# Kernel tuning notes

Measured on AMD Instinct MI355X. Metric: run time of the kernel, lower is better.

The kernel has to match this reference:

```python
import jax, jax.numpy as jnp
import numpy as np

SIGMA = 1.0
BN_EPS = 1e-5
N_OP, N_MACH, N_JOB = 200000, 1000, 20000
E_OM, E_JO, N_PAIRS = 1000000, 200000, 500000
H, D0 = 64, 32


def _bn(x, g, b):
    # BatchNorm1d, training-mode batch statistics over the node/row dim
    m = x.mean(0)
    v = x.var(0)
    return g * (x - m) * jax.lax.rsqrt(v + BN_EPS) + b


def _encode(x, W):
    # MultiPeriodicEncoder: learned frequencies, concat(sin, cos) -> 2*16 = 32 dims
    h = (x @ W) / SIGMA
    return jnp.concatenate([jnp.sin(h), jnp.cos(h)], axis=-1)


def _gin(x_dst, agg, eps, W1, b1, g1, be1, W2, b2):
    # GINConv: MLP((1+eps)*x + sum-aggregated messages); MLP = Lin->BN->ReLU->Lin
    h = ((1.0 + eps) * x_dst + agg) @ W1 + b1
    h = jax.nn.relu(_bn(h, g1, be1))
    return h @ W2 + b2


def _forward(x_operation, x_machine, x_job,
             W_enc_op, W_enc_mach, W_enc_job,
             gin_W1_l0, gin_W1_l12, gin_b1, gin_g1, gin_be1, gin_W2, gin_b2, gin_eps,
             Ws1, bs1, gs1, bes1, Ws2, bs2, gs2, bes2, Ws3, bs3,
             e_om_src, e_om_dst, e_mo_src, e_mo_dst, e_jo_src, e_jo_dst,
             e_oj_src, e_oj_dst, vp_op, vp_mach, vp_job):
    x_op = _encode(x_operation, W_enc_op)    # [N_OP, 32]
    x_ma = _encode(x_machine, W_enc_mach)    # [N_MACH, 32]
    x_jb = _encode(x_job, W_enc_job)         # [N_JOB, 32]
    num_layers = gin_eps.shape[0]
    for l in range(num_layers):
        def p(e):
            W1 = gin_W1_l0[e] if l == 0 else gin_W1_l12[l - 1, e]
            return (gin_eps[l, e], W1, gin_b1[l, e], gin_g1[l, e],
                    gin_be1[l, e], gin_W2[l, e], gin_b2[l, e])
        # edge-type order: 0=op->mach, 1=mach->op, 2=job->op, 3=op->job
        agg_mach = jax.ops.segment_sum(x_op[e_om_src], e_om_dst, num_segments=N_MACH)
        agg_op_mo = jax.ops.segment_sum(x_ma[e_mo_src], e_mo_dst, num_segments=N_OP)
        agg_op_jo = jax.ops.segment_sum(x_jb[e_jo_src], e_jo_dst, num_segments=N_OP)
        agg_job = jax.ops.segment_sum(x_op[e_oj_src], e_oj_dst, num_segments=N_JOB)
        new_ma = _gin(x_ma, agg_mach, *p(0))
        new_op = _gin(x_op, agg_op_mo, *p(1)) + _gin(x_op, agg_op_jo, *p(2))  # hetero 'sum'
        new_jb = _gin(x_jb, agg_job, *p(3))
        if l > 0:  # residual add of previous layer output (= current input)
            new_op = new_op + x_op
            new_ma = new_ma + x_ma
            new_jb = new_jb + x_jb
        x_op, x_ma, x_jb = new_op, new_ma, new_jb
    # gather by valid_pairs, concat in node-type order [operation, machine, job]
    feat = jnp.concatenate([x_op[vp_op], x_ma[vp_mach], x_jb[vp_job]], axis=1)  # [P, 192]
    h = jax.nn.relu(_bn(feat @ Ws1 + bs1, gs1, bes1))
    h = jax.nn.relu(_bn(h @ Ws2 + bs2, gs2, bes2))
    return (h @ Ws3 + bs3)[:, 0]


def setup_inputs() -> dict:
    key = jax.random.key(0)
    ks = jax.random.split(key, 24)
    rn = lambda k, s: jax.random.normal(k, s, dtype=jnp.float32) * 0.1
    return {
        'x_operation': jax.random.normal(ks[0], (N_OP, 8), dtype=jnp.float32),
        'x_machine': jax.random.normal(ks[1], (N_MACH, 4), dtype=jnp.float32),
        'x_job': jax.random.normal(ks[2], (N_JOB, 4), dtype=jnp.float32),
        'W_enc_op': rn(ks[3], (8, 16)),
        'W_enc_mach': rn(ks[4], (4, 16)),
        'W_enc_job': rn(ks[5], (4, 16)),
        'gin_W1_l0': rn(ks[6], (4, D0, H)),
        'gin_W1_l12': rn(ks[7], (2, 4, H, H)),
        'gin_b1': jnp.zeros((3, 4, H), jnp.float32),
        'gin_g1': jnp.ones((3, 4, H), jnp.float32),
        'gin_be1': jnp.zeros((3, 4, H), jnp.float32),
        'gin_W2': rn(ks[8], (3, 4, H, H)),
        'gin_b2': jnp.zeros((3, 4, H), jnp.float32),
        'gin_eps': jnp.zeros((3, 4), jnp.float32),
        'Ws1': rn(ks[9], (3 * H, H)),
        'bs1': jnp.zeros((H,), jnp.float32),
        'gs1': jnp.ones((H,), jnp.float32),
        'bes1': jnp.zeros((H,), jnp.float32),
        'Ws2': rn(ks[10], (H, H // 2)),
        'bs2': jnp.zeros((H // 2,), jnp.float32),
        'gs2': jnp.ones((H // 2,), jnp.float32),
        'bes2': jnp.zeros((H // 2,), jnp.float32),
        'Ws3': rn(ks[11], (H // 2, 1)),
        'bs3': jnp.zeros((1,), jnp.float32),
        'e_om_src': jax.random.randint(ks[12], (E_OM,), 0, N_OP),
        'e_om_dst': jax.random.randint(ks[13], (E_OM,), 0, N_MACH),
        'e_mo_src': jax.random.randint(ks[14], (E_OM,), 0, N_MACH),
        'e_mo_dst': jax.random.randint(ks[15], (E_OM,), 0, N_OP),
        'e_jo_src': jax.random.randint(ks[16], (E_JO,), 0, N_JOB),
        'e_jo_dst': jax.random.randint(ks[17], (E_JO,), 0, N_OP),
        'e_oj_src': jax.random.randint(ks[18], (E_JO,), 0, N_OP),
        'e_oj_dst': jax.random.randint(ks[19], (E_JO,), 0, N_JOB),
        'vp_op': jax.random.randint(ks[20], (N_PAIRS,), 0, N_OP),
        'vp_mach': jax.random.randint(ks[21], (N_PAIRS,), 0, N_MACH),
        'vp_job': jax.random.randint(ks[22], (N_PAIRS,), 0, N_JOB),
    }


def reference(x_operation, x_machine, x_job,
              W_enc_op, W_enc_mach, W_enc_job,
              gin_W1_l0, gin_W1_l12, gin_b1, gin_g1, gin_be1, gin_W2, gin_b2, gin_eps,
              Ws1, bs1, gs1, bes1, Ws2, bs2, gs2, bes2, Ws3, bs3,
              e_om_src, e_om_dst, e_mo_src, e_mo_dst, e_jo_src, e_jo_dst,
              e_oj_src, e_oj_dst, vp_op, vp_mach, vp_job):
    return _forward(x_operation, x_machine, x_job,
                    W_enc_op, W_enc_mach, W_enc_job,
                    gin_W1_l0, gin_W1_l12, gin_b1, gin_g1, gin_be1, gin_W2, gin_b2, gin_eps,
                    Ws1, bs1, gs1, bes1, Ws2, bs2, gs2, bes2, Ws3, bs3,
                    e_om_src, e_om_dst, e_mo_src, e_mo_dst, e_jo_src, e_jo_dst,
                    e_oj_src, e_oj_dst, vp_op, vp_mach, vp_job)
```

## Files before the change

kernel.cpp:

```cpp
#include <hip/hip_runtime.h>
#include <math.h>

#define N_OP_   200000
#define N_MACH_ 1000
#define N_JOB_  20000
#define E_OM_   1000000
#define E_JO_   200000
#define N_PAIRS_ 500000

#define B_OM_ 0
#define B_MO_ 64000
#define B_JO_ 264000
#define B_OJ_ 464000
#define TOTC_ 484000
#define E_TOT_ 2400000

#define CDIV(a,b) (((a)+(b)-1)/(b))

__device__ __forceinline__ unsigned short f2bf(float f){
  unsigned int u = __float_as_uint(f);
  return (unsigned short)((u + 0x7fffu + ((u>>16)&1u)) >> 16);
}
__device__ __forceinline__ float bf2f(unsigned short h){
  return __uint_as_float(((unsigned int)h)<<16);
}

template<int DIN>
__global__ __launch_bounds__(256) void encode_kernel(const float* __restrict__ x,
    const float* __restrict__ W, float* __restrict__ out, int N){
  __shared__ float sW[DIN*16];
  if (threadIdx.x < DIN*16) sW[threadIdx.x] = W[threadIdx.x];
  __syncthreads();
  int i = blockIdx.x*blockDim.x + threadIdx.x;
  if (i >= N) return;
  float xv[DIN];
#pragma unroll
  for (int k=0;k<DIN;k++) xv[k] = x[i*DIN+k];
#pragma unroll
  for (int j=0;j<16;j++){
    float h = 0.f;
#pragma unroll
    for (int k=0;k<DIN;k++) h = fmaf(xv[k], sW[k*16+j], h);
    float s, c;
    sincosf(h, &s, &c);
    out[(size_t)i*64 + j]      = s;
    out[(size_t)i*64 + 16 + j] = c;
  }
}

__device__ __forceinline__ int edge_cidx(int e,
    const int* __restrict__ eom_d, const int* __restrict__ emo_d,
    const int* __restrict__ ejo_d, const int* __restrict__ eoj_d){
  if (e < E_OM_)            return B_OM_ + eom_d[e]*64 + (e & 63);
  else if (e < 2*E_OM_)     return B_MO_ + emo_d[e - E_OM_];
  else if (e < 2*E_OM_+E_JO_) return B_JO_ + ejo_d[e - 2*E_OM_];
  else                      return B_OJ_ + eoj_d[e - 2*E_OM_ - E_JO_];
}
__device__ __forceinline__ int edge_src(int e,
    const int* __restrict__ eom_s, const int* __restrict__ emo_s,
    const int* __restrict__ ejo_s, const int* __restrict__ eoj_s){
  if (e < E_OM_)            return eom_s[e];
  else if (e < 2*E_OM_)     return emo_s[e - E_OM_];
  else if (e < 2*E_OM_+E_JO_) return ejo_s[e - 2*E_OM_];
  else                      return eoj_s[e - 2*E_OM_ - E_JO_];
}

__global__ __launch_bounds__(256) void hist_all_kernel(
    const int* __restrict__ eom_d, const int* __restrict__ emo_d,
    const int* __restrict__ ejo_d, const int* __restrict__ eoj_d,
    int* __restrict__ cnt){
  int gsz = gridDim.x*blockDim.x;
  int i0 = blockIdx.x*blockDim.x + threadIdx.x;
  for (int base = i0; base < E_TOT_; base += 8*gsz){
    int c[8]; bool act[8];
#pragma unroll
    for (int j=0;j<8;j++){
      int e = base + j*gsz;
      act[j] = (e < E_TOT_);
      if (act[j]) c[j] = edge_cidx(e, eom_d, emo_d, ejo_d, eoj_d);
    }
#pragma unroll
    for (int j=0;j<8;j++) if (act[j]) atomicAdd(&cnt[c[j]], 1);
  }
}

__global__ __launch_bounds__(256) void fill_all_kernel(
    const int* __restrict__ eom_s, const int* __restrict__ eom_d,
    const int* __restrict__ emo_s, const int* __restrict__ emo_d,
    const int* __restrict__ ejo_s, const int* __restrict__ ejo_d,
    const int* __restrict__ eoj_s, const int* __restrict__ eoj_d,
    int* __restrict__ cursor, int* __restrict__ elist){
  int gsz = gridDim.x*blockDim.x;
  int i0 = blockIdx.x*blockDim.x + threadIdx.x;
  for (int base = i0; base < E_TOT_; base += 8*gsz){
    int cidx[8], src[8]; bool act[8];
#pragma unroll
    for (int j=0;j<8;j++){
      int e = base + j*gsz;
      act[j] = (e < E_TOT_);
      if (act[j]){
        cidx[j] = edge_cidx(e, eom_d, emo_d, ejo_d, eoj_d);
        src[j]  = edge_src (e, eom_s, emo_s, ejo_s, eoj_s);
      }
    }
    int p[8];
#pragma unroll
    for (int j=0;j<8;j++) if (act[j]) p[j] = atomicAdd(&cursor[cidx[j]], 1);
#pragma unroll
    for (int j=0;j<8;j++) if (act[j]) elist[p[j]] = src[j];
  }
}

__global__ void scan_block_sums(const int* __restrict__ cnt, int N, int* __restrict__ partials){
  __shared__ int red[256];
  int base = blockIdx.x*2048;
  int s = 0;
#pragma unroll
  for (int j=0;j<8;j++){ int i = base + threadIdx.x + j*256; if (i<N) s += cnt[i]; }
  red[threadIdx.x] = s; __syncthreads();
  for (int st=128; st>0; st>>=1){ if (threadIdx.x<st) red[threadIdx.x]+=red[threadIdx.x+st]; __syncthreads(); }
  if (threadIdx.x==0) partials[blockIdx.x] = red[0];
}

__global__ void scan_partials(int* __restrict__ partials, int NB, int* __restrict__ offN){
  __shared__ int buf[256];
  int v = (threadIdx.x < NB) ? partials[threadIdx.x] : 0;
  buf[threadIdx.x] = v; __syncthreads();
  int acc = v;
  for (int st=1; st<256; st<<=1){
    int t = (threadIdx.x >= st) ? buf[threadIdx.x-st] : 0;
    __syncthreads();
    acc += t; buf[threadIdx.x] = acc;
    __syncthreads();
  }
  if (threadIdx.x < NB) partials[threadIdx.x] = acc - v;
  if (threadIdx.x == NB-1) offN[0] = acc;
}

__global__ void scan_write_offsets(const int* __restrict__ cnt, int N,
    const int* __restrict__ partials, int* __restrict__ off){
  __shared__ int buf[256];
  int base = blockIdx.x*2048;
  int v[8]; int s = 0;
#pragma unroll
  for (int j=0;j<8;j++){ int i = base + threadIdx.x*8 + j; v[j] = (i<N)?cnt[i]:0; s += v[j]; }
  buf[threadIdx.x] = s; __syncthreads();
  int acc = s;
  for (int st=1; st<256; st<<=1){
    int t = (threadIdx.x >= st) ? buf[threadIdx.x-st] : 0;
    __syncthreads();
    acc += t; buf[threadIdx.x] = acc;
    __syncthreads();
  }
  int ex = partials[blockIdx.x] + acc - s;
#pragma unroll
  for (int j=0;j<8;j++){ int i = base + threadIdx.x*8 + j; if (i<N) off[i] = ex; ex += v[j]; }
}

__global__ __launch_bounds__(256) void agg_block_kernel(const int* __restrict__ off,
    const int* __restrict__ srcs, const float* __restrict__ feat,
    float* __restrict__ outp, int Ndst, int D){
  __shared__ float red[4][64];
  int m = blockIdx.x;
  if (m >= Ndst) return;
  int g = threadIdx.x >> 6, lane = threadIdx.x & 63;
  int s = off[m*64], e = off[m*64 + 64];
  float acc = 0.f;
  for (int base = s + g*64; base < e; base += 256){
    int cnt = e - base; if (cnt > 64) cnt = 64;
    int r = (lane < cnt) ? srcs[base + lane] : 0;
    int i = 0;
    for (; i + 4 <= cnt; i += 4){
      int r0 = __shfl(r, i), r1 = __shfl(r, i+1), r2 = __shfl(r, i+2), r3 = __shfl(r, i+3);
      float v0 = feat[(size_t)r0*64 + lane];
      float v1 = feat[(size_t)r1*64 + lane];
      float v2 = feat[(size_t)r2*64 + lane];
      float v3 = feat[(size_t)r3*64 + lane];
      acc += (v0 + v1) + (v2 + v3);
    }
    for (; i < cnt; i++){
      int ri = __shfl(r, i);
      acc += feat[(size_t)ri*64 + lane];
    }
  }
  red[g][lane] = acc;
  __syncthreads();
  if (g==0 && lane<D)
    outp[(size_t)m*64+lane] = red[0][lane]+red[1][lane]+red[2][lane]+red[3][lane];
}

template<int K>
__global__ __launch_bounds__(256,3) void partA_fused_kernel(
    const int* __restrict__ off_all, const int* __restrict__ elist,
    const float* __restrict__ Xop, const float* __restrict__ Xma, const float* __restrict__ Xjb,
    float* hm, float* ho1, float* ho2, float* hj,
    const float* __restrict__ Wm, const float* __restrict__ Wa,
    const float* __restrict__ Wb, const float* __restrict__ Wj,
    const float* __restrict__ bm, const float* __restrict__ ba,
    const float* __restrict__ bb, const float* __restrict__ bj,
    float* __restrict__ lstats,
    const float* __restrict__ epsp, int ebase)
{
  constexpr int KP = K + 4;
  constexpr int NF4 = K/16;
  __shared__ float sW[K][64];
  __shared__ float sZ[64][KP];
  __shared__ float sred[16][64];
  const int tid = threadIdx.x;
  const int lc = tid & 15, lr = tid >> 4;
  const int Tm = (N_MACH_+63)>>6, To = (N_OP_+63)>>6;
  int t = blockIdx.x;
  int seg, tile;
  if (t < Tm){ seg=0; tile=t; }
  else if (t < Tm+To){ seg=1; tile=t-Tm; }
  else if (t < Tm+2*To){ seg=2; tile=t-Tm-To; }
  else { seg=3; tile=t-Tm-2*To; }
  float* z            = seg==0?hm:seg==1?ho1:seg==2?ho2:hj;
  const float* x      = seg==0?Xma:seg==3?Xjb:Xop;
  const float* feat   = seg==0?Xop:seg==1?Xma:seg==2?Xjb:Xop;
  const float* W      = seg==0?Wm:seg==1?Wa:seg==2?Wb:Wj;
  const float* b      = seg==0?bm:seg==1?ba:seg==2?bb:bj;
  const int N         = seg==0?N_MACH_:seg==3?N_JOB_:N_OP_;
  const int* offs     = off_all + (seg==0?B_OM_:seg==1?B_MO_:seg==2?B_JO_:B_OJ_);
  float* st           = lstats + seg*128;
  const float e1 = 1.0f + epsp[ebase + seg];
  for (int idx = tid*4; idx < K*64; idx += 1024){
    int k = idx >> 6, c = idx & 63;
    *(float4*)&sW[k][c] = *(const float4*)&W[(size_t)k*64 + c];
  }
  float4 bias4 = *(const float4*)&b[lc*4];
  const int rbase = tile << 6;
  {
    const int r = tid >> 2, q = tid & 3;
    const int cbase = q*(K/4);
    int row = rbase + r;
    float4 a4[NF4];
#pragma unroll
    for (int f=0; f<NF4; f++) a4[f] = make_float4(0.f,0.f,0.f,0.f);
    if (row < N){
      if (seg == 0){
        const float4* H4 = (const float4*)&z[(size_t)row*64 + cbase];
#pragma unroll
        for (int f=0; f<NF4; f++) a4[f] = H4[f];
      } else {
        int s = offs[row], e = offs[row+1];
        int i = s;
        for (; i+2<=e; i+=2){
          int s0 = elist[i], s1 = elist[i+1];
          const float4* F0 = (const float4*)&feat[(size_t)s0*64 + cbase];
          const float4* F1 = (const float4*)&feat[(size_t)s1*64 + cbase];
          float4 v0[NF4], v1[NF4];
#pragma unroll
          for (int f=0; f<NF4; f++){ v0[f]=F0[f]; v1[f]=F1[f]; }
#pragma unroll
          for (int f=0; f<NF4; f++){
            a4[f].x += v0[f].x + v1[f].x;
            a4[f].y += v0[f].y + v1[f].y;
            a4[f].z += v0[f].z + v1[f].z;
            a4[f].w += v0[f].w + v1[f].w;
          }
        }
        if (i < e){
          int s0 = elist[i];
          const float4* F0 = (const float4*)&feat[(size_t)s0*64 + cbase];
#pragma unroll
          for (int f=0; f<NF4; f++){
            float4 v = F0[f];
            a4[f].x += v.x; a4[f].y += v.y; a4[f].z += v.z; a4[f].w += v.w;
          }
        }
      }
      const float4* X4 = (const float4*)&x[(size_t)row*64 + cbase];
#pragma unroll
      for (int f=0; f<NF4; f++){
        float4 xv = X4[f];
        a4[f].x = fmaf(e1, xv.x, a4[f].x);
        a4[f].y = fmaf(e1, xv.y, a4[f].y);
        a4[f].z = fmaf(e1, xv.z, a4[f].z);
        a4[f].w = fmaf(e1, xv.w, a4[f].w);
      }
    }
#pragma unroll
    for (int f=0; f<NF4; f++) *(float4*)&sZ[r][cbase + f*4] = a4[f];
  }
  __syncthreads();
  float acc[4][4];
#pragma unroll
  for (int i=0;i<4;i++){ acc[i][0]=0.f; acc[i][1]=0.f; acc[i][2]=0.f; acc[i][3]=0.f; }
#pragma unroll 2
  for (int kb = 0; kb < K/4; kb++){
    float4 zf[4], wf[4];
#pragma unroll
    for (int i=0;i<4;i++) zf[i] = *(const float4*)&sZ[lr*4+i][kb*4];
#pragma unroll
    for (int kk=0;kk<4;kk++) wf[kk] = *(const float4*)&sW[kb*4+kk][lc*4];
#pragma unroll
    for (int i=0;i<4;i++){
      acc[i][0] = fmaf(zf[i].x, wf[0].x, acc[i][0]);
      acc[i][1] = fmaf(zf[i].x, wf[0].y, acc[i][1]);
      acc[i][2] = fmaf(zf[i].x, wf[0].z, acc[i][2]);
      acc[i][3] = fmaf(zf[i].x, wf[0].w, acc[i][3]);
      acc[i][0] = fmaf(zf[i].y, wf[1].x, acc[i][0]);
      acc[i][1] = fmaf(zf[i].y, wf[1].y, acc[i][1]);
      acc[i][2] = fmaf(zf[i].y, wf[1].z, acc[i][2]);
      acc[i][3] = fmaf(zf[i].y, wf[1].w, acc[i][3]);
      acc[i][0] = fmaf(zf[i].z, wf[2].x, acc[i][0]);
      acc[i][1] = fmaf(zf[i].z, wf[2].y, acc[i][1]);
      acc[i][2] = fmaf(zf[i].z, wf[2].z, acc[i][2]);
      acc[i][3] = fmaf(zf[i].z, wf[2].w, acc[i][3]);
      acc[i][0] = fmaf(zf[i].w, wf[3].x, acc[i][0]);
      acc[i][1] = fmaf(zf[i].w, wf[3].y, acc[i][1]);
      acc[i][2] = fmaf(zf[i].w, wf[3].z, acc[i][2]);
      acc[i][3] = fmaf(zf[i].w, wf[3].w, acc[i][3]);
    }
  }
  float4 psum = make_float4(0.f,0.f,0.f,0.f), psq = make_float4(0.f,0.f,0.f,0.f);
#pragma unroll
  for (int i=0;i<4;i++){
    int row = rbase + lr*4 + i;
    if (row < N){
      float4 o;
      o.x = acc[i][0] + bias4.x;
      o.y = acc[i][1] + bias4.y;
      o.z = acc[i][2] + bias4.z;
      o.w = acc[i][3] + bias4.w;
      *(float4*)&z[(size_t)row*64 + lc*4] = o;
      psum.x += o.x; psum.y += o.y; psum.z += o.z; psum.w += o.w;
      psq.x += o.x*o.x; psq.y += o.y*o.y; psq.z += o.z*o.z; psq.w += o.w*o.w;
    }
  }
  __syncthreads();
  *(float4*)&sred[lr][lc*4] = psum;
  __syncthreads();
  if (tid < 64){
    float s = 0.f;
#pragma unroll
    for (int j=0;j<16;j++) s += sred[j][tid];
    atomicAdd(&st[tid], s);
  }
  __syncthreads();
  *(float4*)&sred[lr][lc*4] = psq;
  __syncthreads();
  if (tid < 64){
    float s = 0.f;
#pragma unroll
    for (int j=0;j<16;j++) s += sred[j][tid];
    atomicAdd(&st[64+tid], s);
  }
}

template<bool RESID>
__global__ __launch_bounds__(256,3) void partB_batch_kernel(
    float* h0, const float* x0, const float* W20, const float* b20, const float* sc0, int N0,
    float* hA, const float* hBp, const float* x1, const float* W2a, const float* W2b,
    const float* b2a_, const float* b2b_, const float* scA, const float* scB, int N1,
    float* h3, const float* x3, const float* W23, const float* b23, const float* sc3, int N3)
{
  __shared__ float sW[64][64];
  __shared__ float sZ[64][68];
  const int tid = threadIdx.x;
  const int lc = tid & 15, lr = tid >> 4;
  const int T0=(N0+63)>>6, T1=(N1+63)>>6;
  int t = blockIdx.x;
  int seg, tile;
  if (t < T0){ seg=0; tile=t; }
  else if (t < T0+T1){ seg=1; tile=t-T0; }
  else { seg=2; tile=t-T0-T1; }
  const int N = seg==0?N0:seg==1?N1:N3;
  float* hout = seg==0?h0:seg==1?hA:h3;
  const float* x = seg==0?x0:seg==1?x1:x3;
  const int rbase = tile << 6;
  const int nsrc = (seg==1) ? 2 : 1;
  float4 bias4;
  if (seg==1){
    float4 ba4 = *(const float4*)&b2a_[lc*4];
    float4 bb4 = *(const float4*)&b2b_[lc*4];
    bias4 = make_float4(ba4.x+bb4.x, ba4.y+bb4.y, ba4.z+bb4.z, ba4.w+bb4.w);
  } else {
    const float* b = seg==0?b20:b23;
    bias4 = *(const float4*)&b[lc*4];
  }
  float acc[4][4];
#pragma unroll
  for (int i=0;i<4;i++){ acc[i][0]=0.f; acc[i][1]=0.f; acc[i][2]=0.f; acc[i][3]=0.f; }
  for (int s=0; s<nsrc; s++){
    const float* hsrc = (seg==1) ? (s==0? (const float*)hA : hBp)
                                 : (seg==0? (const float*)h0 : (const float*)h3);
    const float* Wp   = (seg==1) ? (s==0? W2a : W2b) : (seg==0? W20 : W23);
    const float* scp  = (seg==1) ? (s==0? scA : scB) : (seg==0? sc0 : sc3);
    __syncthreads();
    for (int idx = tid*4; idx < 4096; idx += 1024){
      int k = idx >> 6, c = idx & 63;
      *(float4*)&sW[k][c] = *(const float4*)&Wp[(size_t)k*64 + c];
    }
    for (int idx = tid*4; idx < 4096; idx += 1024){
      int r = idx >> 6, c = idx & 63;
      int row = rbase + r;
      float4 zv = make_float4(0.f,0.f,0.f,0.f);
      if (row < N){
        float4 hv = *(const float4*)&hsrc[(size_t)row*64 + c];
        float4 sc4 = *(const float4*)&scp[c];
        float4 sh4 = *(const float4*)&scp[64 + c];
        zv.x = fmaf(sc4.x, hv.x, sh4.x); zv.x = zv.x > 0.f ? zv.x : 0.f;
        zv.y = fmaf(sc4.y, hv.y, sh4.y); zv.y = zv.y > 0.f ? zv.y : 0.f;
        zv.z = fmaf(sc4.z, hv.z, sh4.z); zv.z = zv.z > 0.f ? zv.z : 0.f;
        zv.w = fmaf(sc4.w, hv.w, sh4.w); zv.w = zv.w > 0.f ? zv.w : 0.f;
      }
      *(float4*)&sZ[r][c] = zv;
    }
    __syncthreads();
#pragma unroll 2
    for (int kb = 0; kb < 16; kb++){
      float4 zf[4], wf[4];
#pragma unroll
      for (int i=0;i<4;i++) zf[i] = *(const float4*)&sZ[lr*4+i][kb*4];
#pragma unroll
      for (int kk=0;kk<4;kk++) wf[kk] = *(const float4*)&sW[kb*4+kk][lc*4];
#pragma unroll
      for (int i=0;i<4;i++){
        acc[i][0] = fmaf(zf[i].x, wf[0].x, acc[i][0]);
        acc[i][1] = fmaf(zf[i].x, wf[0].y, acc[i][1]);
        acc[i][2] = fmaf(zf[i].x, wf[0].z, acc[i][2]);
        acc[i][3] = fmaf(zf[i].x, wf[0].w, acc[i][3]);
        acc[i][0] = fmaf(zf[i].y, wf[1].x, acc[i][0]);
        acc[i][1] = fmaf(zf[i].y, wf[1].y, acc[i][1]);
        acc[i][2] = fmaf(zf[i].y, wf[1].z, acc[i][2]);
        acc[i][3] = fmaf(zf[i].y, wf[1].w, acc[i][3]);
        acc[i][0] = fmaf(zf[i].z, wf[2].x, acc[i][0]);
        acc[i][1] = fmaf(zf[i].z, wf[2].y, acc[i][1]);
        acc[i][2] = fmaf(zf[i].z, wf[2].z, acc[i][2]);
        acc[i][3] = fmaf(zf[i].z, wf[2].w, acc[i][3]);
        acc[i][0] = fmaf(zf[i].w, wf[3].x, acc[i][0]);
        acc[i][1] = fmaf(zf[i].w, wf[3].y, acc[i][1]);
        acc[i][2] = fmaf(zf[i].w, wf[3].z, acc[i][2]);
        acc[i][3] = fmaf(zf[i].w, wf[3].w, acc[i][3]);
      }
    }
  }
#pragma unroll
  for (int i=0;i<4;i++){
    int row = rbase + lr*4 + i;
    if (row < N){
      float4 o;
      o.x = acc[i][0] + bias4.x;
      o.y = acc[i][1] + bias4.y;
      o.z = acc[i][2] + bias4.z;
      o.w = acc[i][3] + bias4.w;
      if (RESID){
        float4 rv = *(const float4*)&x[(size_t)row*64 + lc*4];
        o.x += rv.x; o.y += rv.y; o.z += rv.z; o.w += rv.w;
      }
      *(float4*)&hout[(size_t)row*64 + lc*4] = o;
    }
  }
}

__global__ __launch_bounds__(256,3) void fp1_gemm_kernel(
    const float* __restrict__ Xop, const float* __restrict__ Xma, const float* __restrict__ Xjb,
    const int* __restrict__ vpo, const int* __restrict__ vpm, const int* __restrict__ vpj,
    const float* __restrict__ Ws1, const float* __restrict__ bs1,
    unsigned short* __restrict__ h1bf,
    int P, float* __restrict__ gsum, float* __restrict__ gsq)
{
  __shared__ float sW[64][64];
  __shared__ float sZ[64][68];
  __shared__ float sred[16][64];
  const int tid = threadIdx.x;
  const int lc = tid & 15, lr = tid >> 4;
  float4 bias4 = *(const float4*)&bs1[lc*4];
  float4 psum = make_float4(0.f,0.f,0.f,0.f), psq = make_float4(0.f,0.f,0.f,0.f);
  const int ntiles = (P + 63) >> 6;
  for (int t = blockIdx.x; t < ntiles; t += gridDim.x){
    const int rbase = t << 6;
    float acc[4][4];
#pragma unroll
    for (int i=0;i<4;i++){ acc[i][0]=0.f; acc[i][1]=0.f; acc[i][2]=0.f; acc[i][3]=0.f; }
    for (int s=0; s<3; s++){
      const int* vps = (s==0) ? vpo : (s==1) ? vpm : vpj;
      const float* Xs = (s==0) ? Xop : (s==1) ? Xma : Xjb;
      __syncthreads();
      for (int idx = tid*4; idx < 4096; idx += 1024){
        int r = idx >> 6, c = idx & 63;
        int row = rbase + r;
        float4 z = make_float4(0.f,0.f,0.f,0.f);
        if (row < P){
          int nd = vps[row];
          z = *(const float4*)&Xs[(size_t)nd*64 + c];
        }
        *(float4*)&sZ[r][c] = z;
      }
      for (int idx = tid*4; idx < 4096; idx += 1024){
        int k = idx >> 6, c = idx & 63;
        *(float4*)&sW[k][c] = *(const float4*)&Ws1[(size_t)(s*64 + k)*64 + c];
      }
      __syncthreads();
#pragma unroll 2
      for (int kb = 0; kb < 16; kb++){
        float4 zf[4], wf[4];
#pragma unroll
        for (int i=0;i<4;i++) zf[i] = *(const float4*)&sZ[lr*4+i][kb*4];
#pragma unroll
        for (int kk=0;kk<4;kk++) wf[kk] = *(const float4*)&sW[kb*4+kk][lc*4];
#pragma unroll
        for (int i=0;i<4;i++){
          acc[i][0] = fmaf(zf[i].x, wf[0].x, acc[i][0]);
          acc[i][1] = fmaf(zf[i].x, wf[0].y, acc[i][1]);
          acc[i][2] = fmaf(zf[i].x, wf[0].z, acc[i][2]);
          acc[i][3] = fmaf(zf[i].x, wf[0].w, acc[i][3]);
          acc[i][0] = fmaf(zf[i].y, wf[1].x, acc[i][0]);
          acc[i][1] = fmaf(zf[i].y, wf[1].y, acc[i][1]);
          acc[i][2] = fmaf(zf[i].y, wf[1].z, acc[i][2]);
          acc[i][3] = fmaf(zf[i].y, wf[1].w, acc[i][3]);
          acc[i][0] = fmaf(zf[i].z, wf[2].x, acc[i][0]);
          acc[i][1] = fmaf(zf[i].z, wf[2].y, acc[i][1]);
          acc[i][2] = fmaf(zf[i].z, wf[2].z, acc[i][2]);
          acc[i][3] = fmaf(zf[i].z, wf[2].w, acc[i][3]);
          acc[i][0] = fmaf(zf[i].w, wf[3].x, acc[i][0]);
          acc[i][1] = fmaf(zf[i].w, wf[3].y, acc[i][1]);
          acc[i][2] = fmaf(zf[i].w, wf[3].z, acc[i][2]);
          acc[i][3] = fmaf(zf[i].w, wf[3].w, acc[i][3]);
        }
      }
    }
#pragma unroll
    for (int i=0;i<4;i++){
      int row = rbase + lr*4 + i;
      if (row < P){
        float4 o;
        o.x = acc[i][0] + bias4.x;
        o.y = acc[i][1] + bias4.y;
        o.z = acc[i][2] + bias4.z;
        o.w = acc[i][3] + bias4.w;
        ushort4 u;
        u.x = f2bf(o.x); u.y = f2bf(o.y); u.z = f2bf(o.z); u.w = f2bf(o.w);
        *(ushort4*)&h1bf[(size_t)row*64 + lc*4] = u;
        psum.x += o.x; psum.y += o.y; psum.z += o.z; psum.w += o.w;
        psq.x += o.x*o.x; psq.y += o.y*o.y; psq.z += o.z*o.z; psq.w += o.w*o.w;
      }
    }
  }
  __syncthreads();
  *(float4*)&sred[lr][lc*4] = psum;
  __syncthreads();
  if (tid < 64){
    float s = 0.f;
#pragma unroll
    for (int j=0;j<16;j++) s += sred[j][tid];
    atomicAdd(&gsum[tid], s);
  }
  __syncthreads();
  *(float4*)&sred[lr][lc*4] = psq;
  __syncthreads();
  if (tid < 64){
    float s = 0.f;
#pragma unroll
    for (int j=0;j<16;j++) s += sred[j][tid];
    atomicAdd(&gsq[tid], s);
  }
}

__global__ __launch_bounds__(256,3) void fp2_lite_kernel(
    const float* __restrict__ scsh1,
    const float* __restrict__ Ws2, const float* __restrict__ bs2,
    const unsigned short* __restrict__ h1bf,
    float* __restrict__ s2out, int P,
    float* __restrict__ gsum2, float* __restrict__ gsq2)
{
  __shared__ float sZ[64][68];
  __shared__ float sW2[64][32];
  __shared__ float sred[16][64];
  const int tid = threadIdx.x;
  const int lc = tid & 15, lr = tid >> 4;
  for (int idx = tid*4; idx < 2048; idx += 1024){
    int k = idx >> 5, c = idx & 31;
    *(float4*)&sW2[k][c] = *(const float4*)&Ws2[(size_t)k*32 + c];
  }
  const float b2a = bs2[lc*2], b2b = bs2[lc*2+1];
  const int rbase = blockIdx.x << 6;
  for (int idx = tid*4; idx < 4096; idx += 1024){
    int r = idx >> 6, c = idx & 63;
    int row = rbase + r;
    float4 a = make_float4(0.f,0.f,0.f,0.f);
    if (row < P){
      ushort4 u = *(const ushort4*)&h1bf[(size_t)row*64 + c];
      float4 sc4 = *(const float4*)&scsh1[c];
      float4 sh4 = *(const float4*)&scsh1[64 + c];
      a.x = fmaf(sc4.x, bf2f(u.x), sh4.x); a.x = a.x > 0.f ? a.x : 0.f;
      a.y = fmaf(sc4.y, bf2f(u.y), sh4.y); a.y = a.y > 0.f ? a.y : 0.f;
      a.z = fmaf(sc4.z, bf2f(u.z), sh4.z); a.z = a.z > 0.f ? a.z : 0.f;
      a.w = fmaf(sc4.w, bf2f(u.w), sh4.w); a.w = a.w > 0.f ? a.w : 0.f;
    }
    *(float4*)&sZ[r][c] = a;
  }
  __syncthreads();
  float a2[4][2];
#pragma unroll
  for (int i=0;i<4;i++){ a2[i][0]=0.f; a2[i][1]=0.f; }
#pragma unroll 2
  for (int kb=0; kb<16; kb++){
    float4 zf[4];
    float2 wf[4];
#pragma unroll
    for (int i=0;i<4;i++) zf[i] = *(const float4*)&sZ[lr*4+i][kb*4];
#pragma unroll
    for (int kk=0;kk<4;kk++) wf[kk] = *(const float2*)&sW2[kb*4+kk][lc*2];
#pragma unroll
    for (int i=0;i<4;i++){
      a2[i][0] = fmaf(zf[i].x, wf[0].x, a2[i][0]);
      a2[i][1] = fmaf(zf[i].x, wf[0].y, a2[i][1]);
      a2[i][0] = fmaf(zf[i].y, wf[1].x, a2[i][0]);
      a2[i][1] = fmaf(zf[i].y, wf[1].y, a2[i][1]);
      a2[i][0] = fmaf(zf[i].z, wf[2].x, a2[i][0]);
      a2[i][1] = fmaf(zf[i].z, wf[2].y, a2[i][1]);
      a2[i][0] = fmaf(zf[i].w, wf[3].x, a2[i][0]);
      a2[i][1] = fmaf(zf[i].w, wf[3].y, a2[i][1]);
    }
  }
  float psum0=0.f, psum1=0.f, psq0=0.f, psq1=0.f;
#pragma unroll
  for (int i=0;i<4;i++){
    int row = rbase + lr*4 + i;
    if (row < P){
      float v0 = a2[i][0] + b2a;
      float v1 = a2[i][1] + b2b;
      *(float2*)&s2out[(size_t)row*32 + lc*2] = make_float2(v0, v1);
      psum0 += v0; psum1 += v1;
      psq0 += v0*v0; psq1 += v1*v1;
    }
  }
  __syncthreads();
  sred[lr][lc*2] = psum0; sred[lr][lc*2+1] = psum1;
  __syncthreads();
  if (tid < 32){
    float s = 0.f;
#pragma unroll
    for (int j=0;j<16;j++) s += sred[j][tid];
    atomicAdd(&gsum2[tid], s);
  }
  __syncthreads();
  sred[lr][lc*2] = psq0; sred[lr][lc*2+1] = psq1;
  __syncthreads();
  if (tid < 32){
    float s = 0.f;
#pragma unroll
    for (int j=0;j<16;j++) s += sred[j][tid];
    atomicAdd(&gsq2[tid], s);
  }
}

__global__ void bn_fin4_kernel(const float* __restrict__ stats,
    const float* __restrict__ g1, const float* __restrict__ be1, int l,
    float* __restrict__ scsh){
  int t = threadIdx.x;
  if (t >= 256) return;
  int gi = t>>6, c = t&63;
  float N = (gi==0) ? 1000.f : (gi==3) ? 20000.f : 200000.f;
  float invN = 1.f/N;
  float s = stats[gi*128 + c];
  float q = stats[gi*128 + 64 + c];
  float m = s*invN;
  float var = q*invN - m*m;
  float inv = rsqrtf(var + 1e-5f);
  float gg = g1[((size_t)l*4+gi)*64 + c];
  float bb = be1[((size_t)l*4+gi)*64 + c];
  float sc = gg*inv;
  scsh[gi*128 + c]      = sc;
  scsh[gi*128 + 64 + c] = bb - m*sc;
}

__global__ void bn_fin_kernel(const float* __restrict__ ssum, const float* __restrict__ ssq,
    const float* __restrict__ g, const float* __restrict__ be, float invN, int C,
    float* __restrict__ scsh){
  int c = threadIdx.x;
  if (c >= C) return;
  float m = ssum[c]*invN;
  float var = ssq[c]*invN - m*m;
  float inv = rsqrtf(var + 1e-5f);
  float s = g[c]*inv;
  scsh[c] = s; scsh[64+c] = be[c] - m*s;
}

__global__ __launch_bounds__(256) void final_pass3_kernel(
    const float* __restrict__ s2, const float* __restrict__ Ws3, const float* __restrict__ bs3,
    const float* __restrict__ scsh2,
    float* __restrict__ outp, int P){
  __shared__ float w3[32], c2[32], h2[32];
  __shared__ float b3;
  if (threadIdx.x < 32){
    w3[threadIdx.x]=Ws3[threadIdx.x];
    c2[threadIdx.x]=scsh2[threadIdx.x];
    h2[threadIdx.x]=scsh2[64+threadIdx.x];
  }
  if (threadIdx.x == 0) b3 = bs3[0];
  __syncthreads();
  int r = blockIdx.x*blockDim.x + threadIdx.x;
  if (r >= P) return;
  float acc = b3;
  const float4* S4 = (const float4*)(s2 + (size_t)r*32);
#pragma unroll
  for (int k4=0;k4<8;k4++){
    float4 v = S4[k4];
    float a;
    a = c2[4*k4+0]*v.x + h2[4*k4+0]; acc += (a>0.f?a:0.f)*w3[4*k4+0];
    a = c2[4*k4+1]*v.y + h2[4*k4+1]; acc += (a>0.f?a:0.f)*w3[4*k4+1];
    a = c2[4*k4+2]*v.z + h2[4*k4+2]; acc += (a>0.f?a:0.f)*w3[4*k4+2];
    a = c2[4*k4+3]*v.w + h2[4*k4+3]; acc += (a>0.f?a:0.f)*w3[4*k4+3];
  }
  outp[r] = acc;
}

extern "C" void kernel_launch(void* const* d_in, const int* in_sizes, int n_in,
                              void* d_out, int out_size, void* d_ws, size_t ws_size,
                              hipStream_t stream){
  (void)in_sizes; (void)n_in; (void)out_size; (void)ws_size;
  const float* x_op   = (const float*)d_in[0];
  const float* x_ma   = (const float*)d_in[1];
  const float* x_jb   = (const float*)d_in[2];
  const float* Wenc_op= (const float*)d_in[3];
  const float* Wenc_ma= (const float*)d_in[4];
  const float* Wenc_jb= (const float*)d_in[5];
  const float* gW1_l0 = (const float*)d_in[6];
  const float* gW1_l12= (const float*)d_in[7];
  const float* gb1    = (const float*)d_in[8];
  const float* gg1    = (const float*)d_in[9];
  const float* gbe1   = (const float*)d_in[10];
  const float* gW2    = (const float*)d_in[11];
  const float* gb2    = (const float*)d_in[12];
  const float* geps   = (const float*)d_in[13];
  const float* Ws1    = (const float*)d_in[14];
  const float* bs1    = (const float*)d_in[15];
  const float* gs1    = (const float*)d_in[16];
  const float* bes1   = (const float*)d_in[17];
  const float* Ws2    = (const float*)d_in[18];
  const float* bs2    = (const float*)d_in[19];
  const float* gs2    = (const float*)d_in[20];
  const float* bes2   = (const float*)d_in[21];
  const float* Ws3    = (const float*)d_in[22];
  const float* bs3    = (const float*)d_in[23];
  const int* eom_s = (const int*)d_in[24];
  const int* eom_d = (const int*)d_in[25];
  const int* emo_s = (const int*)d_in[26];
  const int* emo_d = (const int*)d_in[27];
  const int* ejo_s = (const int*)d_in[28];
  const int* ejo_d = (const int*)d_in[29];
  const int* eoj_s = (const int*)d_in[30];
  const int* eoj_d = (const int*)d_in[31];
  const int* vpo = (const int*)d_in[32];
  const int* vpm = (const int*)d_in[33];
  const int* vpj = (const int*)d_in[34];
  float* outp = (float*)d_out;

  char* wsp = (char*)d_ws;
  auto alloc = [&](size_t bytes)->void*{
    void* p = (void*)wsp;
    wsp += (bytes + 255) & ~(size_t)255;
    return p;
  };
  float* P0 = (float*)alloc((size_t)N_OP_*64*4);
  float* P1 = (float*)alloc((size_t)N_OP_*64*4);
  float* P2 = (float*)alloc((size_t)N_OP_*64*4);
  float* J0 = (float*)alloc((size_t)N_JOB_*64*4);
  float* J1 = (float*)alloc((size_t)N_JOB_*64*4);
  float* M0 = (float*)alloc((size_t)N_MACH_*64*4);
  float* M1 = (float*)alloc((size_t)N_MACH_*64*4);
  float* S2 = (float*)alloc((size_t)N_PAIRS_*32*4);
  int* off_all  = (int*)alloc((size_t)(TOTC_+1)*4);
  int* cnt_all  = (int*)alloc((size_t)TOTC_*4);
  int* elist_all= (int*)alloc((size_t)E_TOT_*4);
  int* partials = (int*)alloc(1024*4);
  float* lstats = (float*)alloc(512*4);
  float* lscsh  = (float*)alloc(512*4);
  float* fstats = (float*)alloc(512*4);

  encode_kernel<8><<<CDIV(N_OP_,256),256,0,stream>>>(x_op, Wenc_op, P0, N_OP_);
  encode_kernel<4><<<CDIV(N_MACH_,256),256,0,stream>>>(x_ma, Wenc_ma, M0, N_MACH_);
  encode_kernel<4><<<CDIV(N_JOB_,256),256,0,stream>>>(x_jb, Wenc_jb, J0, N_JOB_);

  hipMemsetAsync(cnt_all, 0, (size_t)TOTC_*4, stream);
  const int GE = CDIV(E_TOT_/8, 256);
  hist_all_kernel<<<GE,256,0,stream>>>(eom_d, emo_d, ejo_d, eoj_d, cnt_all);
  const int NB = CDIV(TOTC_, 2048);
  scan_block_sums<<<NB,256,0,stream>>>(cnt_all, TOTC_, partials);
  scan_partials<<<1,256,0,stream>>>(partials, NB, off_all + TOTC_);
  scan_write_offsets<<<NB,256,0,stream>>>(cnt_all, TOTC_, partials, off_all);
  hipMemcpyAsync(cnt_all, off_all, (size_t)TOTC_*4, hipMemcpyDeviceToDevice, stream);
  fill_all_kernel<<<GE,256,0,stream>>>(eom_s, eom_d, emo_s, emo_d,
                                       ejo_s, ejo_d, eoj_s, eoj_d,
                                       cnt_all, elist_all);

  float *Xop=P0, *Aop=P1, *Bop=P2;
  float *Xjb=J0, *Ajb=J1;
  float *Xma=M0, *Ama=M1;

  const int TA = CDIV(N_MACH_,64) + 2*CDIV(N_OP_,64) + CDIV(N_JOB_,64);
  const int TB = CDIV(N_MACH_,64) + CDIV(N_OP_,64) + CDIV(N_JOB_,64);

  for (int l=0; l<3; l++){
    int Din = (l==0) ? 32 : 64;
    hipMemsetAsync(lstats, 0, 512*4, stream);
    const float *W1m, *W1a, *W1b, *W1j;
    if (l==0){
      W1m = gW1_l0 + (size_t)0*32*64; W1a = gW1_l0 + (size_t)1*32*64;
      W1b = gW1_l0 + (size_t)2*32*64; W1j = gW1_l0 + (size_t)3*32*64;
    } else {
      W1m = gW1_l12 + ((size_t)(l-1)*4+0)*64*64; W1a = gW1_l12 + ((size_t)(l-1)*4+1)*64*64;
      W1b = gW1_l12 + ((size_t)(l-1)*4+2)*64*64; W1j = gW1_l12 + ((size_t)(l-1)*4+3)*64*64;
    }
    const float* b1m = gb1 + ((size_t)l*4+0)*64; const float* b1a = gb1 + ((size_t)l*4+1)*64;
    const float* b1b = gb1 + ((size_t)l*4+2)*64; const float* b1j = gb1 + ((size_t)l*4+3)*64;
    agg_block_kernel<<<N_MACH_,256,0,stream>>>(off_all + B_OM_, elist_all, Xop, Ama, N_MACH_, Din);
    if (l==0){
      partA_fused_kernel<32><<<TA,256,0,stream>>>(
        off_all, elist_all, Xop, Xma, Xjb,
        Ama, Aop, Bop, Ajb,
        W1m, W1a, W1b, W1j, b1m, b1a, b1b, b1j,
        lstats, geps, 0);
    } else {
      partA_fused_kernel<64><<<TA,256,0,stream>>>(
        off_all, elist_all, Xop, Xma, Xjb,
        Ama, Aop, Bop, Ajb,
        W1m, W1a, W1b, W1j, b1m, b1a, b1b, b1j,
        lstats, geps, l*4);
    }
    bn_fin4_kernel<<<1,256,0,stream>>>(lstats, gg1, gbe1, l, lscsh);
    const float* W2m = gW2 + ((size_t)l*4+0)*64*64; const float* b2m = gb2 + ((size_t)l*4+0)*64;
    const float* W2a = gW2 + ((size_t)l*4+1)*64*64; const float* b2a = gb2 + ((size_t)l*4+1)*64;
    const float* W2b = gW2 + ((size_t)l*4+2)*64*64; const float* b2b = gb2 + ((size_t)l*4+2)*64;
    const float* W2j = gW2 + ((size_t)l*4+3)*64*64; const float* b2j = gb2 + ((size_t)l*4+3)*64;
    if (l==0){
      partB_batch_kernel<false><<<TB,256,0,stream>>>(
        Ama, Xma, W2m, b2m, lscsh+0,   N_MACH_,
        Aop, Bop, Xop, W2a, W2b, b2a, b2b, lscsh+128, lscsh+256, N_OP_,
        Ajb, Xjb, W2j, b2j, lscsh+384, N_JOB_);
    } else {
      partB_batch_kernel<true><<<TB,256,0,stream>>>(
        Ama, Xma, W2m, b2m, lscsh+0,   N_MACH_,
        Aop, Bop, Xop, W2a, W2b, b2a, b2b, lscsh+128, lscsh+256, N_OP_,
        Ajb, Xjb, W2j, b2j, lscsh+384, N_JOB_);
    }
    { float* t=Xma; Xma=Ama; Ama=t; }
    { float* t=Xop; Xop=Aop; Aop=t; }
    { float* t=Xjb; Xjb=Ajb; Ajb=t; }
  }

  float* fsum1 = fstats;       float* fsq1 = fstats+64;
  float* fsum2 = fstats+128;   float* fsq2 = fstats+192;
  float* scsh1 = fstats+256;
  float* scsh2 = fstats+384;
  unsigned short* H1BF = (unsigned short*)S2;
  hipMemsetAsync(fstats, 0, 256*4, stream);
  fp1_gemm_kernel<<<2048,256,0,stream>>>(Xop,Xma,Xjb,vpo,vpm,vpj,Ws1,bs1,H1BF,N_PAIRS_,fsum1,fsq1);
  bn_fin_kernel<<<1,64,0,stream>>>(fsum1,fsq1,gs1,bes1, 1.f/(float)N_PAIRS_, 64, scsh1);
  fp2_lite_kernel<<<CDIV(N_PAIRS_,64),256,0,stream>>>(scsh1, Ws2, bs2, H1BF, S2, N_PAIRS_, fsum2, fsq2);
  bn_fin_kernel<<<1,32,0,stream>>>(fsum2,fsq2,gs2,bes2, 1.f/(float)N_PAIRS_, 32, scsh2);
  final_pass3_kernel<<<CDIV(N_PAIRS_,256),256,0,stream>>>(S2, Ws3, bs3, scsh2, outp, N_PAIRS_);
}
```

Measured before the change: 1.471 ms.

## Use bf16 MFMA instructions for second-layer GIN and pair-scoring GEMMs

Replaces the scalar fp32 FMA inner loops in partB_batch_kernel and fp1_gemm_kernel with 16x16x32 bf16 MFMA matrix instructions. Activations and weights are converted to bf16 when staged into shared memory, and the weights are stored transposed. The output epilogue now writes scalar elements per the MFMA accumulator layout instead of float4 vectors, and the BN statistics reduction is remapped to match. This lowers precision of these GEMMs to bf16 inputs and makes the output stores less coalesced, in exchange for offloading the arithmetic to matrix cores.

```diff
diff --git a/kernel.cpp b/kernel.cpp
--- a/kernel.cpp
+++ b/kernel.cpp
@@ -16,6 +16,9 @@
 #define E_TOT_ 2400000
 
 #define CDIV(a,b) (((a)+(b)-1)/(b))
+
+typedef __attribute__((ext_vector_type(8))) short short8v;
+typedef __attribute__((ext_vector_type(4))) float f32x4;
 
 __device__ __forceinline__ unsigned short f2bf(float f){
   unsigned int u = __float_as_uint(f);
@@ -356,10 +359,11 @@
     const float* b2a_, const float* b2b_, const float* scA, const float* scB, int N1,
     float* h3, const float* x3, const float* W23, const float* b23, const float* sc3, int N3)
 {
-  __shared__ float sW[64][64];
-  __shared__ float sZ[64][68];
+  __shared__ unsigned short sA[64][72];
+  __shared__ unsigned short sB[64][72];
   const int tid = threadIdx.x;
-  const int lc = tid & 15, lr = tid >> 4;
+  const int lane = tid & 63, w = tid >> 6;
+  const int lo = lane & 15, hi = lane >> 4;
   const int T0=(N0+63)>>6, T1=(N1+63)>>6;
   int t = blockIdx.x;
   int seg, tile;
@@ -371,86 +375,65 @@
   const float* x = seg==0?x0:seg==1?x1:x3;
   const int rbase = tile << 6;
   const int nsrc = (seg==1) ? 2 : 1;
-  float4 bias4;
-  if (seg==1){
-    float4 ba4 = *(const float4*)&b2a_[lc*4];
-    float4 bb4 = *(const float4*)&b2b_[lc*4];
-    bias4 = make_float4(ba4.x+bb4.x, ba4.y+bb4.y, ba4.z+bb4.z, ba4.w+bb4.w);
-  } else {
-    const float* b = seg==0?b20:b23;
-    bias4 = *(const float4*)&b[lc*4];
-  }
-  float acc[4][4];
-#pragma unroll
-  for (int i=0;i<4;i++){ acc[i][0]=0.f; acc[i][1]=0.f; acc[i][2]=0.f; acc[i][3]=0.f; }
+  f32x4 acc[4];
+#pragma unroll
+  for (int n=0;n<4;n++) acc[n] = (f32x4){0.f,0.f,0.f,0.f};
   for (int s=0; s<nsrc; s++){
     const float* hsrc = (seg==1) ? (s==0? (const float*)hA : hBp)
                                  : (seg==0? (const float*)h0 : (const float*)h3);
     const float* Wp   = (seg==1) ? (s==0? W2a : W2b) : (seg==0? W20 : W23);
     const float* scp  = (seg==1) ? (s==0? scA : scB) : (seg==0? sc0 : sc3);
     __syncthreads();
-    for (int idx = tid*4; idx < 4096; idx += 1024){
-      int k = idx >> 6, c = idx & 63;
-      *(float4*)&sW[k][c] = *(const float4*)&Wp[(size_t)k*64 + c];
-    }
-    for (int idx = tid*4; idx < 4096; idx += 1024){
-      int r = idx >> 6, c = idx & 63;
+    for (int idx = tid; idx < 1024; idx += 256){
+      int k = idx >> 4, c4 = (idx & 15)*4;
+      float4 wv = *(const float4*)&Wp[(size_t)k*64 + c4];
+      sB[c4+0][k] = f2bf(wv.x);
+      sB[c4+1][k] = f2bf(wv.y);
+      sB[c4+2][k] = f2bf(wv.z);
+      sB[c4+3][k] = f2bf(wv.w);
+    }
+    for (int idx = tid; idx < 1024; idx += 256){
+      int r = idx >> 4, c4 = (idx & 15)*4;
       int row = rbase + r;
-      float4 zv = make_float4(0.f,0.f,0.f,0.f);
+      ushort4 zz = make_ushort4(0,0,0,0);
       if (row < N){
-        float4 hv = *(const float4*)&hsrc[(size_t)row*64 + c];
-        float4 sc4 = *(const float4*)&scp[c];
-        float4 sh4 = *(const float4*)&scp[64 + c];
-        zv.x = fmaf(sc4.x, hv.x, sh4.x); zv.x = zv.x > 0.f ? zv.x : 0.f;
-        zv.y = fmaf(sc4.y, hv.y, sh4.y); zv.y = zv.y > 0.f ? zv.y : 0.f;
-        zv.z = fmaf(sc4.z, hv.z, sh4.z); zv.z = zv.z > 0.f ? zv.z : 0.f;
-        zv.w = fmaf(sc4.w, hv.w, sh4.w); zv.w = zv.w > 0.f ? zv.w : 0.f;
+        float4 hv = *(const float4*)&hsrc[(size_t)row*64 + c4];
+        float4 sc4 = *(const float4*)&scp[c4];
+        float4 sh4 = *(const float4*)&scp[64 + c4];
+        float a0 = fmaf(sc4.x, hv.x, sh4.x); a0 = a0>0.f?a0:0.f;
+        float a1 = fmaf(sc4.y, hv.y, sh4.y); a1 = a1>0.f?a1:0.f;
+        float a2 = fmaf(sc4.z, hv.z, sh4.z); a2 = a2>0.f?a2:0.f;
+        float a3 = fmaf(sc4.w, hv.w, sh4.w); a3 = a3>0.f?a3:0.f;
+        zz = make_ushort4(f2bf(a0), f2bf(a1), f2bf(a2), f2bf(a3));
       }
-      *(float4*)&sZ[r][c] = zv;
+      *(ushort4*)&sA[r][c4] = zz;
     }
     __syncthreads();
-#pragma unroll 2
-    for (int kb = 0; kb < 16; kb++){
-      float4 zf[4], wf[4];
-#pragma unroll
-      for (int i=0;i<4;i++) zf[i] = *(const float4*)&sZ[lr*4+i][kb*4];
-#pragma unroll
-      for (int kk=0;kk<4;kk++) wf[kk] = *(const float4*)&sW[kb*4+kk][lc*4];
-#pragma unroll
-      for (int i=0;i<4;i++){
-        acc[i][0] = fmaf(zf[i].x, wf[0].x, acc[i][0]);
-        acc[i][1] = fmaf(zf[i].x, wf[0].y, acc[i][1]);
-        acc[i][2] = fmaf(zf[i].x, wf[0].z, acc[i][2]);
-        acc[i][3] = fmaf(zf[i].x, wf[0].w, acc[i][3]);
-        acc[i][0] = fmaf(zf[i].y, wf[1].x, acc[i][0]);
-        acc[i][1] = fmaf(zf[i].y, wf[1].y, acc[i][1]);
-        acc[i][2] = fmaf(zf[i].y, wf[1].z, acc[i][2]);
-        acc[i][3] = fmaf(zf[i].y, wf[1].w, acc[i][3]);
-        acc[i][0] = fmaf(zf[i].z, wf[2].x, acc[i][0]);
-        acc[i][1] = fmaf(zf[i].z, wf[2].y, acc[i][1]);
-        acc[i][2] = fmaf(zf[i].z, wf[2].z, acc[i][2]);
-        acc[i][3] = fmaf(zf[i].z, wf[2].w, acc[i][3]);
-        acc[i][0] = fmaf(zf[i].w, wf[3].x, acc[i][0]);
-        acc[i][1] = fmaf(zf[i].w, wf[3].y, acc[i][1]);
-        acc[i][2] = fmaf(zf[i].w, wf[3].z, acc[i][2]);
-        acc[i][3] = fmaf(zf[i].w, wf[3].w, acc[i][3]);
+    short8v af0 = *(const short8v*)&sA[w*16 + lo][hi*8];
+    short8v af1 = *(const short8v*)&sA[w*16 + lo][32 + hi*8];
+#pragma unroll
+    for (int n=0;n<4;n++){
+      short8v bf0 = *(const short8v*)&sB[n*16 + lo][hi*8];
+      short8v bf1 = *(const short8v*)&sB[n*16 + lo][32 + hi*8];
+      acc[n] = __builtin_amdgcn_mfma_f32_16x16x32_bf16(af0, bf0, acc[n], 0, 0, 0);
+      acc[n] = __builtin_amdgcn_mfma_f32_16x16x32_bf16(af1, bf1, acc[n], 0, 0, 0);
+    }
+  }
+#pragma unroll
+  for (int n=0;n<4;n++){
+    int col = n*16 + lo;
+    float bv;
+    if (seg==1) bv = b2a_[col] + b2b_[col];
+    else if (seg==0) bv = b20[col];
+    else bv = b23[col];
+#pragma unroll
+    for (int j=0;j<4;j++){
+      int row = rbase + w*16 + hi*4 + j;
+      if (row < N){
+        float v = acc[n][j] + bv;
+        if (RESID) v += x[(size_t)row*64 + col];
+        hout[(size_t)row*64 + col] = v;
       }
-    }
-  }
-#pragma unroll
-  for (int i=0;i<4;i++){
-    int row = rbase + lr*4 + i;
-    if (row < N){
-      float4 o;
-      o.x = acc[i][0] + bias4.x;
-      o.y = acc[i][1] + bias4.y;
-      o.z = acc[i][2] + bias4.z;
-      o.w = acc[i][3] + bias4.w;
-      if (RESID){
-        float4 rv = *(const float4*)&x[(size_t)row*64 + lc*4];
-        o.x += rv.x; o.y += rv.y; o.z += rv.z; o.w += rv.w;
-      }
-      *(float4*)&hout[(size_t)row*64 + lc*4] = o;
     }
   }
 }
@@ -462,85 +445,72 @@
     unsigned short* __restrict__ h1bf,
     int P, float* __restrict__ gsum, float* __restrict__ gsq)
 {
-  __shared__ float sW[64][64];
-  __shared__ float sZ[64][68];
+  __shared__ unsigned short sA[64][72];
+  __shared__ unsigned short sB[64][72];
   __shared__ float sred[16][64];
   const int tid = threadIdx.x;
-  const int lc = tid & 15, lr = tid >> 4;
-  float4 bias4 = *(const float4*)&bs1[lc*4];
-  float4 psum = make_float4(0.f,0.f,0.f,0.f), psq = make_float4(0.f,0.f,0.f,0.f);
+  const int lane = tid & 63, w = tid >> 6;
+  const int lo = lane & 15, hi = lane >> 4;
+  float ps[4] = {0.f,0.f,0.f,0.f};
+  float pq[4] = {0.f,0.f,0.f,0.f};
   const int ntiles = (P + 63) >> 6;
   for (int t = blockIdx.x; t < ntiles; t += gridDim.x){
     const int rbase = t << 6;
-    float acc[4][4];
-#pragma unroll
-    for (int i=0;i<4;i++){ acc[i][0]=0.f; acc[i][1]=0.f; acc[i][2]=0.f; acc[i][3]=0.f; }
+    f32x4 acc[4];
+#pragma unroll
+    for (int n=0;n<4;n++) acc[n] = (f32x4){0.f,0.f,0.f,0.f};
     for (int s=0; s<3; s++){
       const int* vps = (s==0) ? vpo : (s==1) ? vpm : vpj;
       const float* Xs = (s==0) ? Xop : (s==1) ? Xma : Xjb;
       __syncthreads();
-      for (int idx = tid*4; idx < 4096; idx += 1024){
-        int r = idx >> 6, c = idx & 63;
+      for (int idx = tid; idx < 1024; idx += 256){
+        int k = idx >> 4, c4 = (idx & 15)*4;
+        float4 wv = *(const float4*)&Ws1[(size_t)(s*64 + k)*64 + c4];
+        sB[c4+0][k] = f2bf(wv.x);
+        sB[c4+1][k] = f2bf(wv.y);
+        sB[c4+2][k] = f2bf(wv.z);
+        sB[c4+3][k] = f2bf(wv.w);
+      }
+      for (int idx = tid; idx < 1024; idx += 256){
+        int r = idx >> 4, c4 = (idx & 15)*4;
         int row = rbase + r;
-        float4 z = make_float4(0.f,0.f,0.f,0.f);
+        ushort4 zz = make_ushort4(0,0,0,0);
         if (row < P){
           int nd = vps[row];
-          z = *(const float4*)&Xs[(size_t)nd*64 + c];
+          float4 z = *(const float4*)&Xs[(size_t)nd*64 + c4];
+          zz = make_ushort4(f2bf(z.x), f2bf(z.y), f2bf(z.z), f2bf(z.w));
         }
-        *(float4*)&sZ[r][c] = z;
-      }
-      for (int idx = tid*4; idx < 4096; idx += 1024){
-        int k = idx >> 6, c = idx & 63;
-        *(float4*)&sW[k][c] = *(const float4*)&Ws1[(size_t)(s*64 + k)*64 + c];
+        *(ushort4*)&sA[r][c4] = zz;
       }
       __syncthreads();
-#pragma unroll 2
-      for (int kb = 0; kb < 16; kb++){
-        float4 zf[4], wf[4];
-#pragma unroll
-        for (int i=0;i<4;i++) zf[i] = *(const float4*)&sZ[lr*4+i][kb*4];
-#pragma unroll
-        for (int kk=0;kk<4;kk++) wf[kk] = *(const float4*)&sW[kb*4+kk][lc*4];
-#pragma unroll
-        for (int i=0;i<4;i++){
-          acc[i][0] = fmaf(zf[i].x, wf[0].x, acc[i][0]);
-          acc[i][1] = fmaf(zf[i].x, wf[0].y, acc[i][1]);
-          acc[i][2] = fmaf(zf[i].x, wf[0].z, acc[i][2]);
-          acc[i][3] = fmaf(zf[i].x, wf[0].w, acc[i][3]);
-          acc[i][0] = fmaf(zf[i].y, wf[1].x, acc[i][0]);
-          acc[i][1] = fmaf(zf[i].y, wf[1].y, acc[i][1]);
-          acc[i][2] = fmaf(zf[i].y, wf[1].z, acc[i][2]);
-          acc[i][3] = fmaf(zf[i].y, wf[1].w, acc[i][3]);
-          acc[i][0] = fmaf(zf[i].z, wf[2].x, acc[i][0]);
-          acc[i][1] = fmaf(zf[i].z, wf[2].y, acc[i][1]);
-          acc[i][2] = fmaf(zf[i].z, wf[2].z, acc[i][2]);
-          acc[i][3] = fmaf(zf[i].z, wf[2].w, acc[i][3]);
-          acc[i][0] = fmaf(zf[i].w, wf[3].x, acc[i][0]);
-          acc[i][1] = fmaf(zf[i].w, wf[3].y, acc[i][1]);
-          acc[i][2] = fmaf(zf[i].w, wf[3].z, acc[i][2]);
-          acc[i][3] = fmaf(zf[i].w, wf[3].w, acc[i][3]);
+      short8v af0 = *(const short8v*)&sA[w*16 + lo][hi*8];
+      short8v af1 = *(const short8v*)&sA[w*16 + lo][32 + hi*8];
+#pragma unroll
+      for (int n=0;n<4;n++){
+        short8v bf0 = *(const short8v*)&sB[n*16 + lo][hi*8];
+        short8v bf1 = *(const short8v*)&sB[n*16 + lo][32 + hi*8];
+        acc[n] = __builtin_amdgcn_mfma_f32_16x16x32_bf16(af0, bf0, acc[n], 0, 0, 0);
+        acc[n] = __builtin_amdgcn_mfma_f32_16x16x32_bf16(af1, bf1, acc[n], 0, 0, 0);
+      }
+    }
+#pragma unroll
+    for (int n=0;n<4;n++){
+      int col = n*16 + lo;
+      float bv = bs1[col];
+#pragma unroll
+      for (int j=0;j<4;j++){
+        int row = rbase + w*16 + hi*4 + j;
+        if (row < P){
+          float v = acc[n][j] + bv;
+          h1bf[(size_t)row*64 + col] = f2bf(v);
+          ps[n] += v; pq[n] += v*v;
         }
       }
     }
-#pragma unroll
-    for (int i=0;i<4;i++){
-      int row = rbase + lr*4 + i;
-      if (row < P){
-        float4 o;
-        o.x = acc[i][0] + bias4.x;
-        o.y = acc[i][1] + bias4.y;
-        o.z = acc[i][2] + bias4.z;
-        o.w = acc[i][3] + bias4.w;
-        ushort4 u;
-        u.x = f2bf(o.x); u.y = f2bf(o.y); u.z = f2bf(o.z); u.w = f2bf(o.w);
-        *(ushort4*)&h1bf[(size_t)row*64 + lc*4] = u;
-        psum.x += o.x; psum.y += o.y; psum.z += o.z; psum.w += o.w;
-        psq.x += o.x*o.x; psq.y += o.y*o.y; psq.z += o.z*o.z; psq.w += o.w*o.w;
-      }
-    }
-  }
-  __syncthreads();
-  *(float4*)&sred[lr][lc*4] = psum;
+  }
+  __syncthreads();
+#pragma unroll
+  for (int n=0;n<4;n++) sred[w*4 + hi][n*16 + lo] = ps[n];
   __syncthreads();
   if (tid < 64){
     float s = 0.f;
@@ -549,7 +519,8 @@
     atomicAdd(&gsum[tid], s);
   }
   __syncthreads();
-  *(float4*)&sred[lr][lc*4] = psq;
+#pragma unroll
+  for (int n=0;n<4;n++) sred[w*4 + hi][n*16 + lo] = pq[n];
   __syncthreads();
   if (tid < 64){
     float s = 0.f;
```

Measured after the change: 1.370 ms (median of 2 runs). 1.07x faster.
